# Kernel optimization log

Hardware: AMD Instinct MI355X
Metric: run time of the kernel (lower is better)

## Reference

```python
import jax, jax.numpy as jnp
import numpy as np

B, S, H = 2, 2048, 2048
N = 16               # num heads
NOPE, ROPE, V = 128, 64, 128
QHD = NOPE + ROPE    # 192 per-head q/k dim
QL, KVL = 1536, 512  # q_lora_rank, kv_lora_rank
THETA = 10000.0
SCALE = QHD ** -0.5
EPS = 1e-6


def rmsnorm(x, w):
    var = jnp.mean(x.astype(jnp.float32) ** 2, axis=-1, keepdims=True)
    return (x.astype(jnp.float32) * jax.lax.rsqrt(var + EPS)).astype(x.dtype) * w


def rotate_half(x):
    d = x.shape[-1] // 2
    return jnp.concatenate([-x[..., d:], x[..., :d]], axis=-1)


def setup_inputs() -> dict:
    key = jax.random.key(0)
    ks = jax.random.split(key, 8)
    w = lambda k, shape: jax.random.normal(k, shape, jnp.float32) * 0.02
    return {
        "hidden_states": jax.random.normal(ks[0], (B, S, H), jnp.float32),
        "position_ids": (jnp.arange(B * S, dtype=jnp.int64) % 4096).reshape(B, S),
        "q_a_w": w(ks[1], (QL, H)),
        "q_a_ln_w": jnp.ones((QL,), jnp.float32),
        "q_b_w": w(ks[2], (N * QHD, QL)),
        "kv_a_w": w(ks[3], (KVL + ROPE, H)),
        "kv_a_ln_w": jnp.ones((KVL,), jnp.float32),
        "kv_b_w": w(ks[4], (N * (NOPE + V), KVL)),
        "o_w": w(ks[5], (H, N * V)),
    }


def mla_forward(hidden_states, position_ids, q_a_w, q_a_ln_w, q_b_w,
                kv_a_w, kv_a_ln_w, kv_b_w, o_w):
    b, s, _ = hidden_states.shape
    # ---- Q low-rank path: q_b(rmsnorm(q_a(x))) ----
    q = rmsnorm(hidden_states @ q_a_w.T, q_a_ln_w) @ q_b_w.T
    q = q.reshape(b, s, N, QHD)
    q_nope, q_pe = q[..., :NOPE], q[..., NOPE:]
    # ---- compressed KV + shared rope key ----
    kv_a = hidden_states @ kv_a_w.T                       # [b,s,KVL+ROPE]
    compressed_kv = rmsnorm(kv_a[..., :KVL], kv_a_ln_w)   # [b,s,KVL]
    k_pe = kv_a[..., KVL:].reshape(b, s, 1, ROPE)         # MQA rope key
    # ---- RoPE (default, theta=1e4) from position_ids ----
    inv_freq = 1.0 / (THETA ** (jnp.arange(0, ROPE, 2, dtype=jnp.float32) / ROPE))
    freqs = position_ids.astype(jnp.float32)[..., None] * inv_freq  # [b,s,ROPE/2]
    emb = jnp.concatenate([freqs, freqs], axis=-1)                  # [b,s,ROPE]
    cos = jnp.cos(emb)[:, :, None, :].astype(hidden_states.dtype)   # [b,s,1,ROPE]
    sin = jnp.sin(emb)[:, :, None, :].astype(hidden_states.dtype)
    q_pe = q_pe * cos + rotate_half(q_pe) * sin
    k_pe = k_pe * cos + rotate_half(k_pe) * sin
    # ---- decompress latent KV via kv_b_proj ----
    kv = (compressed_kv @ kv_b_w.T).reshape(b, s, N, NOPE + V)
    k_nope, v = kv[..., :NOPE], kv[..., NOPE:]
    k = jnp.concatenate([k_nope, jnp.broadcast_to(k_pe, (b, s, N, ROPE))], axis=-1)
    qf = jnp.concatenate([q_nope, q_pe], axis=-1)          # [b,s,N,QHD]
    # ---- causal SDPA in bsnd layout ----
    scores = jnp.einsum('bqnd,bknd->bnqk', qf, k) * SCALE  # [b,N,s,s]
    causal = jnp.tril(jnp.ones((s, s), bool))
    scores = jnp.where(causal, scores, jnp.finfo(scores.dtype).min)
    probs = jax.nn.softmax(scores, axis=-1)
    attn = jnp.einsum('bnqk,bknd->bqnd', probs, v)         # [b,s,N,V]
    out = attn.reshape(b, s, N * V) @ o_w.T
    return out


def reference(hidden_states, position_ids, q_a_w, q_a_ln_w, q_b_w,
              kv_a_w, kv_a_ln_w, kv_b_w, o_w):
    return mla_forward(hidden_states, position_ids, q_a_w, q_a_ln_w, q_b_w,
                       kv_a_w, kv_a_ln_w, kv_b_w, o_w)
```

## Files before the change

### kernel.cpp

```cpp
#include <hip/hip_runtime.h>
#include <cstdio>

typedef unsigned short u16;
typedef u16 u16x8 __attribute__((ext_vector_type(8)));
typedef __bf16 bf16x8 __attribute__((ext_vector_type(8)));
typedef float f32x4 __attribute__((ext_vector_type(4)));

#define AS1 __attribute__((address_space(1)))
#define AS3 __attribute__((address_space(3)))

#define GLOAD16(gsrc, ldst) __builtin_amdgcn_global_load_lds( \
    (const AS1 void*)(gsrc), (AS3 void*)(ldst), 16, 0, 0)

__device__ __forceinline__ u16 f2bf(float f) {
  unsigned u = __builtin_bit_cast(unsigned, f);
  u += 0x7fffu + ((u >> 16) & 1u);
  return (u16)(u >> 16);
}
__device__ __forceinline__ float bf2f(u16 h) {
  return __builtin_bit_cast(float, (unsigned)h << 16);
}

__global__ __launch_bounds__(256) void cvt_pad_k(const float* __restrict__ src,
                                                 u16* __restrict__ dst,
                                                 long srcN, long dstN) {
  long i = ((long)blockIdx.x * 256 + threadIdx.x) * 8;
  const long stride = (long)gridDim.x * 256 * 8;
  for (; i < dstN; i += stride) {
    u16x8 o = {0,0,0,0,0,0,0,0};
    if (i < srcN) {
      const float4* p = (const float4*)(src + i);
      float4 a = p[0], b = p[1];
      o[0]=f2bf(a.x); o[1]=f2bf(a.y); o[2]=f2bf(a.z); o[3]=f2bf(a.w);
      o[4]=f2bf(b.x); o[5]=f2bf(b.y); o[6]=f2bf(b.z); o[7]=f2bf(b.w);
    }
    *(u16x8*)(dst + i) = o;
  }
}

__global__ __launch_bounds__(256) void rms_k(const u16* __restrict__ src, u16* __restrict__ dst,
                                             const float* __restrict__ w,
                                             int sstride, int dstride, int cols) {
  const int row = blockIdx.x;
  const int tid = threadIdx.x;
  const int nch = cols >> 3;
  float x[8];
  float ss = 0.f;
  if (tid < nch) {
    u16x8 v = *(const u16x8*)(src + (size_t)row * sstride + tid * 8);
#pragma unroll
    for (int j = 0; j < 8; ++j) { x[j] = bf2f(v[j]); ss += x[j] * x[j]; }
  } else {
#pragma unroll
    for (int j = 0; j < 8; ++j) x[j] = 0.f;
  }
#pragma unroll
  for (int off = 1; off < 64; off <<= 1) ss += __shfl_xor(ss, off);
  __shared__ float red[4];
  const int wv = tid >> 6, ln = tid & 63;
  if (ln == 0) red[wv] = ss;
  __syncthreads();
  const float tot = red[0] + red[1] + red[2] + red[3];
  const float rs = 1.0f / sqrtf(tot / (float)cols + 1e-6f);
  if (tid < nch) {
    u16x8 o;
#pragma unroll
    for (int j = 0; j < 8; ++j) o[j] = f2bf(x[j] * rs * w[tid * 8 + j]);
    *(u16x8*)(dst + (size_t)row * dstride + tid * 8) = o;
  }
}

__global__ __launch_bounds__(256) void rope_k(u16* __restrict__ q, const u16* __restrict__ kva,
                                              u16* __restrict__ kpe, const int* __restrict__ pos) {
  const int tok = blockIdx.x;
  const int j = threadIdx.x & 63;
  const int w = threadIdx.x >> 6;
  const float p = (float)pos[tok];
  const int jj = j & 31;
  const float inv = __powf(10000.0f, -(float)jj * (1.0f / 32.0f));
  float s, c;
  __sincosf(p * inv, &s, &c);
  const float sgn = (j < 32) ? -1.0f : 1.0f;
  const int partner = (j < 32) ? j + 32 : j - 32;
  if (w == 0) {
    const float x  = bf2f(kva[(size_t)tok * 640 + 512 + j]);
    const float xp = bf2f(kva[(size_t)tok * 640 + 512 + partner]);
    kpe[(size_t)tok * 64 + j] = f2bf(x * c + sgn * xp * s);
  }
#pragma unroll
  for (int hh = 0; hh < 4; ++hh) {
    const int h = w * 4 + hh;
    const size_t base = (size_t)tok * 3072 + h * 192 + 128;
    const float x  = bf2f(q[base + j]);
    const float xp = bf2f(q[base + partner]);
    q[base + j] = f2bf(x * c + sgn * xp * s);
  }
}

__global__ __launch_bounds__(256) void gemm_bt(const u16* __restrict__ A, const u16* __restrict__ B,
                                               u16* __restrict__ Cb, float* __restrict__ Cf,
                                               int M, int N, int K) {
  __shared__ __attribute__((aligned(16))) u16 As[128 * 64];
  __shared__ __attribute__((aligned(16))) u16 Bs[128 * 64];
  const int tid = threadIdx.x;
  const int m0 = blockIdx.y * 128, n0 = blockIdx.x * 128;
  const int w = tid >> 6, lane = tid & 63;
  const int wr = w >> 1, wc = w & 1;
  const int lr = lane & 15, g = lane >> 4;

  f32x4 acc[4][4] = {};

  for (int k0 = 0; k0 < K; k0 += 64) {
#pragma unroll
    for (int i = 0; i < 4; ++i) {
      const int c = i * 256 + tid;
      const int row = c >> 3, col = (c & 7) << 3;
      GLOAD16(A + (size_t)(m0 + row) * K + k0 + col, &As[c * 8]);
    }
#pragma unroll
    for (int i = 0; i < 4; ++i) {
      const int c = i * 256 + tid;
      const int row = c >> 3, col = (c & 7) << 3;
      GLOAD16(B + (size_t)(n0 + row) * K + k0 + col, &Bs[c * 8]);
    }
    __syncthreads();
    bf16x8 af[4][2], bfr[4][2];
#pragma unroll
    for (int x = 0; x < 4; ++x)
#pragma unroll
      for (int kk = 0; kk < 2; ++kk) {
        af[x][kk]  = *(const bf16x8*)(&As[(wr * 64 + x * 16 + lr) * 64 + kk * 32 + g * 8]);
        bfr[x][kk] = *(const bf16x8*)(&Bs[(wc * 64 + x * 16 + lr) * 64 + kk * 32 + g * 8]);
      }
#pragma unroll
    for (int mi = 0; mi < 4; ++mi)
#pragma unroll
      for (int ni = 0; ni < 4; ++ni)
#pragma unroll
        for (int kk = 0; kk < 2; ++kk)
          acc[mi][ni] = __builtin_amdgcn_mfma_f32_16x16x32_bf16(af[mi][kk], bfr[ni][kk],
                                                                acc[mi][ni], 0, 0, 0);
    __syncthreads();
  }

  const int rb = m0 + wr * 64, cb = n0 + wc * 64;
#pragma unroll
  for (int mi = 0; mi < 4; ++mi)
#pragma unroll
    for (int ni = 0; ni < 4; ++ni)
#pragma unroll
      for (int i = 0; i < 4; ++i) {
        const int r = rb + mi * 16 + g * 4 + i;
        const int cI = cb + ni * 16 + lr;
        if (Cf) Cf[(size_t)r * N + cI] = acc[mi][ni][i];
        else    Cb[(size_t)r * N + cI] = f2bf(acc[mi][ni][i]);
      }
}

__global__ __launch_bounds__(256) void vtr_k(const u16* __restrict__ kvb, u16* __restrict__ vT) {
  __shared__ u16 tile[128 * 72];
  const int bh = blockIdx.x, b = bh >> 4, h = bh & 15;
  const int s0 = blockIdx.y * 64;
  const int t = threadIdx.x;
  {
    const int s = t >> 2;
    const int vc = (t & 3) * 32;
    const u16* src = kvb + (size_t)(b * 2048 + s0 + s) * 4096 + h * 256 + 128 + vc;
#pragma unroll
    for (int c = 0; c < 4; ++c) {
      u16x8 v = *(const u16x8*)(src + c * 8);
#pragma unroll
      for (int e = 0; e < 8; ++e) tile[(vc + c * 8 + e) * 72 + s] = v[e];
    }
  }
  __syncthreads();
  {
    const int v = t >> 1;
    const int sh = (t & 1) * 32;
    u16* dst = vT + (size_t)(bh * 128 + v) * 2048 + s0 + sh;
    const u16* srow = &tile[v * 72 + sh];
#pragma unroll
    for (int c = 0; c < 4; ++c)
      *(u16x8*)(dst + c * 8) = *(const u16x8*)(srow + c * 8);
  }
}

__global__ __launch_bounds__(256) void attn_k(const u16* __restrict__ q, const u16* __restrict__ kvb,
                                              const u16* __restrict__ kpe, const u16* __restrict__ vT,
                                              u16* __restrict__ ao) {
  __shared__ __attribute__((aligned(16))) u16 Ks[64 * 192];
  __shared__ __attribute__((aligned(16))) u16 Vt[128 * 64];

  const float SCALE = 0.07216878364870323f;
  const int bh = blockIdx.x;
  const int b = bh >> 4, h = bh & 15;
  const int j = 15 - blockIdx.y;
  const int tid = threadIdx.x, w = tid >> 6, lane = tid & 63;
  const int lr = lane & 15, g = lane >> 4;

  const int q0 = j * 128;
  const int qrb = q0 + w * 32;
  u16* Psw = &Ks[w * 2304];

  bf16x8 qf[2][6];
#pragma unroll
  for (int m = 0; m < 2; ++m)
#pragma unroll
    for (int kd = 0; kd < 6; ++kd)
      qf[m][kd] = *(const bf16x8*)(q + (size_t)(b * 2048 + qrb + m * 16 + lr) * 3072 +
                                   h * 192 + kd * 32 + g * 8);

  float mrow[2][4], lrow[2][4];
  f32x4 o[2][8] = {};
#pragma unroll
  for (int m = 0; m < 2; ++m)
#pragma unroll
    for (int i = 0; i < 4; ++i) { mrow[m][i] = -1e30f; lrow[m][i] = 0.f; }

  const int nt = (q0 >> 6) + 2;
  for (int t = 0; t < nt; ++t) {
    const int k0 = t * 64;
#pragma unroll
    for (int i = 0; i < 6; ++i) {
      const int c = i * 256 + tid;
      const int row = c / 24, cl = c - row * 24;
      const int cg = cl ^ (row & 7);
      const u16* src = (cg < 16)
        ? (kvb + (size_t)(b * 2048 + k0 + row) * 4096 + h * 256 + cg * 8)
        : (kpe + (size_t)(b * 2048 + k0 + row) * 64 + (cg - 16) * 8);
      GLOAD16(src, &Ks[c * 8]);
    }
#pragma unroll
    for (int i = 0; i < 4; ++i) {
      const int c = i * 256 + tid;
      const int v = c >> 3, cl = c & 7;
      const int cg = cl ^ (v & 7);
      GLOAD16(vT + (size_t)(bh * 128 + v) * 2048 + k0 + cg * 8, &Vt[c * 8]);
    }
    __syncthreads();

    const bool active = (k0 <= qrb + 31);
    f32x4 sAcc[2][4] = {};
    if (active) {
#pragma unroll
      for (int nf = 0; nf < 4; ++nf) {
        const int rr = nf * 16 + lr;
#pragma unroll
        for (int kd = 0; kd < 6; ++kd) {
          const int ch = (kd * 4 + g) ^ (rr & 7);
          const bf16x8 kf = *(const bf16x8*)(&Ks[rr * 192 + ch * 8]);
#pragma unroll
          for (int m = 0; m < 2; ++m)
            sAcc[m][nf] = __builtin_amdgcn_mfma_f32_16x16x32_bf16(qf[m][kd], kf, sAcc[m][nf], 0, 0, 0);
        }
      }
    }
    __syncthreads();

    if (active) {
#pragma unroll
      for (int m = 0; m < 2; ++m) {
        float sv[4][4];
#pragma unroll
        for (int nf = 0; nf < 4; ++nf)
#pragma unroll
          for (int i = 0; i < 4; ++i) {
            const int qrow = qrb + m * 16 + g * 4 + i;
            const int kcol = k0 + nf * 16 + lr;
            const float vS = sAcc[m][nf][i] * SCALE;
            sv[nf][i] = (kcol > qrow) ? -1e30f : vS;
          }
        float fac[4], mn[4];
#pragma unroll
        for (int i = 0; i < 4; ++i) {
          float rm = fmaxf(fmaxf(sv[0][i], sv[1][i]), fmaxf(sv[2][i], sv[3][i]));
          rm = fmaxf(rm, __shfl_xor(rm, 1));
          rm = fmaxf(rm, __shfl_xor(rm, 2));
          rm = fmaxf(rm, __shfl_xor(rm, 4));
          rm = fmaxf(rm, __shfl_xor(rm, 8));
          mn[i] = fmaxf(mrow[m][i], rm);
          fac[i] = __expf(mrow[m][i] - mn[i]);
          mrow[m][i] = mn[i];
        }
#pragma unroll
        for (int i = 0; i < 4; ++i) {
          float rsum = 0.f;
#pragma unroll
          for (int nf = 0; nf < 4; ++nf) { sv[nf][i] = __expf(sv[nf][i] - mn[i]); rsum += sv[nf][i]; }
          rsum += __shfl_xor(rsum, 1);
          rsum += __shfl_xor(rsum, 2);
          rsum += __shfl_xor(rsum, 4);
          rsum += __shfl_xor(rsum, 8);
          lrow[m][i] = lrow[m][i] * fac[i] + rsum;
        }
#pragma unroll
        for (int nv = 0; nv < 8; ++nv)
#pragma unroll
          for (int i = 0; i < 4; ++i) o[m][nv][i] *= fac[i];
#pragma unroll
        for (int nf = 0; nf < 4; ++nf)
#pragma unroll
          for (int i = 0; i < 4; ++i)
            Psw[(m * 16 + g * 4 + i) * 72 + nf * 16 + lr] = f2bf(sv[nf][i]);
      }
      asm volatile("s_waitcnt lgkmcnt(0)" ::: "memory");

#pragma unroll
      for (int kc = 0; kc < 2; ++kc) {
        bf16x8 vfr[8];
#pragma unroll
        for (int nv = 0; nv < 8; ++nv) {
          const int v = nv * 16 + lr;
          const int cx = (kc * 4 + g) ^ (v & 7);
          vfr[nv] = *(const bf16x8*)(&Vt[v * 64 + cx * 8]);
        }
#pragma unroll
        for (int m = 0; m < 2; ++m) {
          const bf16x8 pf = *(const bf16x8*)(&Psw[(m * 16 + lr) * 72 + kc * 32 + g * 8]);
#pragma unroll
          for (int nv = 0; nv < 8; ++nv)
            o[m][nv] = __builtin_amdgcn_mfma_f32_16x16x32_bf16(pf, vfr[nv], o[m][nv], 0, 0, 0);
        }
      }
    }
    __syncthreads();
  }

#pragma unroll
  for (int m = 0; m < 2; ++m)
#pragma unroll
    for (int i = 0; i < 4; ++i) {
      const float inv = 1.0f / lrow[m][i];
      const size_t tokOff = (size_t)(b * 2048 + qrb + m * 16 + g * 4 + i) * 2048 + h * 128;
#pragma unroll
      for (int nv = 0; nv < 8; ++nv)
        ao[tokOff + nv * 16 + lr] = f2bf(o[m][nv][i] * inv);
    }
}

extern "C" void kernel_launch(void* const* d_in, const int* in_sizes, int n_in,
                              void* d_out, int out_size, void* d_ws, size_t ws_size,
                              hipStream_t stream) {
  const float* hidden  = (const float*)d_in[0];
  const int*   pos     = (const int*)d_in[1];
  const float* q_a_w   = (const float*)d_in[2];
  const float* q_a_ln  = (const float*)d_in[3];
  const float* q_b_w   = (const float*)d_in[4];
  const float* kv_a_w  = (const float*)d_in[5];
  const float* kv_a_ln = (const float*)d_in[6];
  const float* kv_b_w  = (const float*)d_in[7];
  const float* o_w     = (const float*)d_in[8];
  float* out = (float*)d_out;

  char* ws = (char*)d_ws;
  u16* hb  = (u16*)(ws + 0L);
  u16* w1  = (u16*)(ws + 16777216L);
  u16* w2  = (u16*)(ws + 23068672L);
  u16* w3  = (u16*)(ws + 32505856L);
  u16* w4  = (u16*)(ws + 35127296L);
  u16* w5  = (u16*)(ws + 39321600L);
  u16* qa  = (u16*)(ws + 47710208L);
  u16* qb  = (u16*)(ws + 60293120L);
  u16* kva = (u16*)(ws + 85458944L);
  u16* ckv = (u16*)(ws + 90701824L);
  u16* kpe = (u16*)(ws + 94896128L);
  u16* kvb = (u16*)(ws + 95420416L);
  u16* ao  = (u16*)(ws + 128974848L);
  u16* vT  = hb;
  if (ws_size < 145752064UL) { fprintf(stderr, "ws too small: %zu\n", ws_size); return; }

  auto cvt = [&](const float* s, u16* d, long sn, long dn) {
    long blocks = (dn / 8 + 255) / 256; if (blocks > 2048) blocks = 2048;
    cvt_pad_k<<<dim3((unsigned)blocks), dim3(256), 0, stream>>>(s, d, sn, dn);
  };
  cvt(hidden, hb, 4096L * 2048, 4096L * 2048);
  cvt(q_a_w,  w1, 1536L * 2048, 1536L * 2048);
  cvt(q_b_w,  w2, 3072L * 1536, 3072L * 1536);
  cvt(kv_a_w, w3, 576L * 2048,  640L * 2048);
  cvt(kv_b_w, w4, 4096L * 512,  4096L * 512);
  cvt(o_w,    w5, 2048L * 2048, 2048L * 2048);

  gemm_bt<<<dim3(12, 32), 256, 0, stream>>>(hb, w1, qa, nullptr, 4096, 1536, 2048);
  rms_k<<<4096, 256, 0, stream>>>(qa, qa, q_a_ln, 1536, 1536, 1536);
  gemm_bt<<<dim3(24, 32), 256, 0, stream>>>(qa, w2, qb, nullptr, 4096, 3072, 1536);
  gemm_bt<<<dim3(5, 32), 256, 0, stream>>>(hb, w3, kva, nullptr, 4096, 640, 2048);
  rms_k<<<4096, 256, 0, stream>>>(kva, ckv, kv_a_ln, 640, 512, 512);
  rope_k<<<4096, 256, 0, stream>>>(qb, kva, kpe, pos);
  gemm_bt<<<dim3(32, 32), 256, 0, stream>>>(ckv, w4, kvb, nullptr, 4096, 4096, 512);
  vtr_k<<<dim3(32, 32), 256, 0, stream>>>(kvb, vT);
  attn_k<<<dim3(32, 16), 256, 0, stream>>>(qb, kvb, kpe, vT, ao);
  gemm_bt<<<dim3(16, 32), 256, 0, stream>>>(ao, w5, nullptr, out, 4096, 2048, 2048);
}
```

Before: 474.9 us.

## Add 256x256-tile double-buffered GEMM kernel for the large projections

```diff
diff --git a/kernel.cpp b/kernel.cpp
--- a/kernel.cpp
+++ b/kernel.cpp
@@ -157,6 +157,105 @@
       }
 }
 
+__global__ __launch_bounds__(512) void gemm256(const u16* __restrict__ A, const u16* __restrict__ B,
+                                               u16* __restrict__ Cb, float* __restrict__ Cf,
+                                               int M, int N, int K) {
+  __shared__ __attribute__((aligned(16))) u16 As[2][256 * 64];
+  __shared__ __attribute__((aligned(16))) u16 Bs[2][256 * 64];
+  const int tid = threadIdx.x;
+  const int m0 = blockIdx.y * 256, n0 = blockIdx.x * 256;
+  const int wid = tid >> 6, lane = tid & 63;
+  const int wr = wid >> 2, wc = wid & 3;
+  const int lr = lane & 15, g = lane >> 4;
+
+  const u16* pA[4];
+  const u16* pB[4];
+  int lOff[4];
+#pragma unroll
+  for (int i = 0; i < 4; ++i) {
+    const int c = i * 512 + tid;
+    const int row = c >> 3, cl = c & 7;
+    const int cg = cl ^ (row & 7);
+    lOff[i] = c * 8;
+    pA[i] = A + (size_t)(m0 + row) * K + cg * 8;
+    pB[i] = B + (size_t)(n0 + row) * K + cg * 8;
+  }
+
+  const int aBase = (wr * 128 + lr) * 64;
+  const int bBase = (wc * 64 + lr) * 64;
+  int kch[2];
+#pragma unroll
+  for (int kk = 0; kk < 2; ++kk) kch[kk] = ((kk * 4 + g) ^ (lr & 7)) * 8;
+
+  f32x4 acc[8][4] = {};
+  const int nkt = K >> 6;
+
+#pragma unroll
+  for (int i = 0; i < 4; ++i) GLOAD16(pA[i], &As[0][lOff[i]]);
+#pragma unroll
+  for (int i = 0; i < 4; ++i) GLOAD16(pB[i], &Bs[0][lOff[i]]);
+#pragma unroll
+  for (int i = 0; i < 4; ++i) { pA[i] += 64; pB[i] += 64; }
+  asm volatile("s_waitcnt vmcnt(0)" ::: "memory");
+  __builtin_amdgcn_s_barrier();
+  __builtin_amdgcn_sched_barrier(0);
+
+  for (int t = 0; t < nkt; ++t) {
+    const int buf = t & 1;
+    if (t + 1 < nkt) {
+#pragma unroll
+      for (int i = 0; i < 4; ++i) GLOAD16(pA[i], &As[buf ^ 1][lOff[i]]);
+#pragma unroll
+      for (int i = 0; i < 4; ++i) GLOAD16(pB[i], &Bs[buf ^ 1][lOff[i]]);
+#pragma unroll
+      for (int i = 0; i < 4; ++i) { pA[i] += 64; pB[i] += 64; }
+    }
+    bf16x8 bfr[4][2];
+#pragma unroll
+    for (int fn = 0; fn < 4; ++fn)
+#pragma unroll
+      for (int kk = 0; kk < 2; ++kk)
+        bfr[fn][kk] = *(const bf16x8*)(&Bs[buf][bBase + fn * 1024 + kch[kk]]);
+#pragma unroll
+    for (int q = 0; q < 4; ++q) {
+      bf16x8 afr[2][2];
+#pragma unroll
+      for (int fr = 0; fr < 2; ++fr)
+#pragma unroll
+        for (int kk = 0; kk < 2; ++kk)
+          afr[fr][kk] = *(const bf16x8*)(&As[buf][aBase + (q * 2 + fr) * 1024 + kch[kk]]);
+      asm volatile("s_waitcnt lgkmcnt(0)" ::: "memory");
+      __builtin_amdgcn_sched_barrier(0);
+      __builtin_amdgcn_s_setprio(1);
+#pragma unroll
+      for (int fr = 0; fr < 2; ++fr)
+#pragma unroll
+        for (int fn = 0; fn < 4; ++fn)
+#pragma unroll
+          for (int kk = 0; kk < 2; ++kk)
+            acc[q * 2 + fr][fn] = __builtin_amdgcn_mfma_f32_16x16x32_bf16(
+                afr[fr][kk], bfr[fn][kk], acc[q * 2 + fr][fn], 0, 0, 0);
+      __builtin_amdgcn_s_setprio(0);
+      if (q == 3) asm volatile("s_waitcnt vmcnt(0)" ::: "memory");
+      __builtin_amdgcn_s_barrier();
+    }
+    __builtin_amdgcn_sched_barrier(0);
+  }
+
+  const int rb = m0 + wr * 128, cb = n0 + wc * 64;
+#pragma unroll
+  for (int fm = 0; fm < 8; ++fm)
+#pragma unroll
+    for (int fn = 0; fn < 4; ++fn)
+#pragma unroll
+      for (int i = 0; i < 4; ++i) {
+        const int r = rb + fm * 16 + g * 4 + i;
+        const int cI = cb + fn * 16 + lr;
+        if (Cf) Cf[(size_t)r * N + cI] = acc[fm][fn][i];
+        else    Cb[(size_t)r * N + cI] = f2bf(acc[fm][fn][i]);
+      }
+}
+
 __global__ __launch_bounds__(256) void vtr_k(const u16* __restrict__ kvb, u16* __restrict__ vT) {
   __shared__ u16 tile[128 * 72];
   const int bh = blockIdx.x, b = bh >> 4, h = bh & 15;
@@ -382,12 +481,12 @@
 
   gemm_bt<<<dim3(12, 32), 256, 0, stream>>>(hb, w1, qa, nullptr, 4096, 1536, 2048);
   rms_k<<<4096, 256, 0, stream>>>(qa, qa, q_a_ln, 1536, 1536, 1536);
-  gemm_bt<<<dim3(24, 32), 256, 0, stream>>>(qa, w2, qb, nullptr, 4096, 3072, 1536);
+  gemm256<<<dim3(12, 16), 512, 0, stream>>>(qa, w2, qb, nullptr, 4096, 3072, 1536);
   gemm_bt<<<dim3(5, 32), 256, 0, stream>>>(hb, w3, kva, nullptr, 4096, 640, 2048);
   rms_k<<<4096, 256, 0, stream>>>(kva, ckv, kv_a_ln, 640, 512, 512);
   rope_k<<<4096, 256, 0, stream>>>(qb, kva, kpe, pos);
-  gemm_bt<<<dim3(32, 32), 256, 0, stream>>>(ckv, w4, kvb, nullptr, 4096, 4096, 512);
+  gemm256<<<dim3(16, 16), 512, 0, stream>>>(ckv, w4, kvb, nullptr, 4096, 4096, 512);
   vtr_k<<<dim3(32, 32), 256, 0, stream>>>(kvb, vT);
   attn_k<<<dim3(32, 16), 256, 0, stream>>>(qb, kvb, kpe, vT, ao);
-  gemm_bt<<<dim3(16, 32), 256, 0, stream>>>(ao, w5, nullptr, out, 4096, 2048, 2048);
-}
+  gemm256<<<dim3(8, 16), 512, 0, stream>>>(ao, w5, nullptr, out, 4096, 2048, 2048);
+}
```

After: 471.9 us. About the same (-0.6%).
